# Performance work log

Measured on AMD Instinct MI355X. Metric: run time of the kernel, lower is better.

## Reference

```python
import jax, jax.numpy as jnp
import numpy as np

B, T, I, H = 256, 256, 2048, 128

def setup_inputs() -> dict:
    key = jax.random.key(0)
    ks = jax.random.split(key, 7)
    s = 1.0 / np.sqrt(H)  # torch RNN/Linear init scale
    return {
        "x": jax.random.normal(ks[0], (B, T, I), dtype=jnp.float32),
        "W_ih": jax.random.uniform(ks[1], (H, I), jnp.float32, -s, s),
        "W_hh": jax.random.uniform(ks[2], (H, H), jnp.float32, -s, s),
        "b_ih": jax.random.uniform(ks[3], (H,), jnp.float32, -s, s),
        "b_hh": jax.random.uniform(ks[4], (H,), jnp.float32, -s, s),
        "W_fc": jax.random.uniform(ks[5], (1, H), jnp.float32, -s, s),
        "b_fc": jax.random.uniform(ks[6], (1,), jnp.float32, -s, s),
    }

def reference(x, W_ih, W_hh, b_ih, b_hh, W_fc, b_fc):
    # Precompute input projection for all timesteps as one big GEMM: [B,T,H]
    xp = jnp.einsum('bti,hi->bth', x, W_ih) + (b_ih + b_hh)
    h0 = jnp.zeros((x.shape[0], W_hh.shape[0]), dtype=x.dtype)

    def step(h, xt):  # xt: [B,H]
        h = jnp.tanh(xt + h @ W_hh.T)
        return h, None

    hT, _ = jax.lax.scan(step, h0, jnp.swapaxes(xp, 0, 1))  # final hidden [B,H]
    out = hT @ W_fc.T + b_fc  # [B,1]
    return out.squeeze(1)     # [B]
```

## Files before the change

### kernel.cpp

```cpp
#include <hip/hip_runtime.h>
#include <hip/hip_bf16.h>
#include <math.h>

#define B_ 256
#define T_ 256
#define I_ 2048
#define H_ 128

#define BM 128
#define BK 32
#define NKT (I_ / BK)

typedef __attribute__((ext_vector_type(8))) short bf16x8;
typedef __attribute__((ext_vector_type(4))) float f32x4;
typedef _Float16 half2v __attribute__((ext_vector_type(2)));

static __device__ inline short f2bf(float f) {
    __hip_bfloat16 h = __float2bfloat16(f);
    return *reinterpret_cast<short*>(&h);
}

static __device__ inline bf16x8 pack8(float4 a, float4 b) {
    bf16x8 r;
    r[0] = f2bf(a.x); r[1] = f2bf(a.y); r[2] = f2bf(a.z); r[3] = f2bf(a.w);
    r[4] = f2bf(b.x); r[5] = f2bf(b.y); r[6] = f2bf(b.z); r[7] = f2bf(b.w);
    return r;
}

#define LGKM_BARRIER() do {                                  \
    asm volatile("s_waitcnt lgkmcnt(0)" ::: "memory");       \
    __builtin_amdgcn_sched_barrier(0);                       \
    __builtin_amdgcn_s_barrier();                            \
} while (0)

__global__ __launch_bounds__(256, 2) void proj_mfma(
    const float* __restrict__ x, const float* __restrict__ Wih,
    const float* __restrict__ bih, const float* __restrict__ bhh,
    float* __restrict__ xp)
{
    __shared__ __align__(16) float As[2][BM * BK];
    __shared__ __align__(16) float Bs[2][H_ * BK];

    const int tid  = threadIdx.x;
    const int lane = tid & 63;
    const int wid  = tid >> 6;
    const int wr   = wid >> 1;
    const int wc   = wid & 1;
    const long row0 = (long)blockIdx.x * BM;

    const int srow  = lane >> 3;
    const int sunit = (lane & 7) ^ srow;

    f32x4 acc[4][4];
    #pragma unroll
    for (int m = 0; m < 4; ++m)
        #pragma unroll
        for (int n = 0; n < 4; ++n)
            acc[m][n] = (f32x4){0.f, 0.f, 0.f, 0.f};

    const int fr = lane & 15;
    const int fq = lane >> 4;
    const int rb0 = wid * 32;

    #pragma unroll
    for (int i = 0; i < 4; ++i) {
        const int rbase = rb0 + i * 8;
        const float* ga = x   + (row0 + rbase + srow) * I_ + sunit * 4;
        const float* gb = Wih + (long)(rbase + srow) * I_ + sunit * 4;
        __builtin_amdgcn_global_load_lds(
            (const __attribute__((address_space(1))) void*)ga,
            (__attribute__((address_space(3))) void*)&As[0][rbase * BK], 16, 0, 0);
        __builtin_amdgcn_global_load_lds(
            (const __attribute__((address_space(1))) void*)gb,
            (__attribute__((address_space(3))) void*)&Bs[0][rbase * BK], 16, 0, 0);
    }
    __syncthreads();

    int p = 0;
    for (int t = 0; t < NKT; ++t) {
        if (t + 1 < NKT) {
            const int kk = (t + 1) * BK;
            #pragma unroll
            for (int i = 0; i < 4; ++i) {
                const int rbase = rb0 + i * 8;
                const float* ga = x   + (row0 + rbase + srow) * I_ + kk + sunit * 4;
                const float* gb = Wih + (long)(rbase + srow) * I_ + kk + sunit * 4;
                __builtin_amdgcn_global_load_lds(
                    (const __attribute__((address_space(1))) void*)ga,
                    (__attribute__((address_space(3))) void*)&As[p ^ 1][rbase * BK], 16, 0, 0);
                __builtin_amdgcn_global_load_lds(
                    (const __attribute__((address_space(1))) void*)gb,
                    (__attribute__((address_space(3))) void*)&Bs[p ^ 1][rbase * BK], 16, 0, 0);
            }
        }
        bf16x8 af[4], bfr[4];
        #pragma unroll
        for (int f = 0; f < 4; ++f) {
            const int ra_ = wr * 64 + f * 16 + fr;
            const float4 a0 = *reinterpret_cast<const float4*>(
                &As[p][ra_ * BK + (((fq * 2)     ^ (ra_ & 7)) * 4)]);
            const float4 a1 = *reinterpret_cast<const float4*>(
                &As[p][ra_ * BK + (((fq * 2 + 1) ^ (ra_ & 7)) * 4)]);
            af[f] = pack8(a0, a1);
            const int rb_ = wc * 64 + f * 16 + fr;
            const float4 b0 = *reinterpret_cast<const float4*>(
                &Bs[p][rb_ * BK + (((fq * 2)     ^ (rb_ & 7)) * 4)]);
            const float4 b1 = *reinterpret_cast<const float4*>(
                &Bs[p][rb_ * BK + (((fq * 2 + 1) ^ (rb_ & 7)) * 4)]);
            bfr[f] = pack8(b0, b1);
        }
        #pragma unroll
        for (int m = 0; m < 4; ++m)
            #pragma unroll
            for (int n = 0; n < 4; ++n)
                acc[m][n] = __builtin_amdgcn_mfma_f32_16x16x32_bf16(
                    af[m], bfr[n], acc[m][n], 0, 0, 0);
        __syncthreads();
        p ^= 1;
    }

    #pragma unroll
    for (int n = 0; n < 4; ++n) {
        const int col = wc * 64 + n * 16 + fr;
        const float bn = bih[col] + bhh[col];
        #pragma unroll
        for (int m = 0; m < 4; ++m) {
            const long rbase = row0 + wr * 64 + m * 16 + fq * 4;
            #pragma unroll
            for (int j = 0; j < 4; ++j)
                xp[(rbase + j) * H_ + col] = acc[m][n][j] + bn;
        }
    }
}

__global__ __launch_bounds__(256) void scan_kernel(
    const float* __restrict__ xp, const float* __restrict__ Whh,
    const float* __restrict__ Wfc, const float* __restrict__ bfc,
    float* __restrict__ out)
{
    __shared__ __align__(16) unsigned hpk[2][H_ / 2];

    const int tid  = threadIdx.x;
    const int lane = tid & 63;
    const int w    = tid >> 6;
    const int j    = w * 32 + (lane & 31);
    const int g    = lane >> 5;
    const int b    = blockIdx.x;

    half2v Wh[32];
    {
        const float4* wp = reinterpret_cast<const float4*>(&Whh[(long)j * H_ + g * 64]);
        #pragma unroll
        for (int q = 0; q < 16; ++q) {
            const float4 wv = wp[q];
            half2v p0, p1;
            p0[0] = (_Float16)wv.x; p0[1] = (_Float16)wv.y;
            p1[0] = (_Float16)wv.z; p1[1] = (_Float16)wv.w;
            Wh[2 * q]     = p0;
            Wh[2 * q + 1] = p1;
        }
    }
    if (tid < H_ / 2) hpk[0][tid] = 0u;

    const float* xprow = xp + (long)b * T_ * H_ + j;
    float xa = xprow[0 * H_];
    float xb = xprow[1 * H_];
    float xc = xprow[2 * H_];
    float xd = xprow[3 * H_];
    __syncthreads();

    auto body = [&](int t, float xpv) {
        const uint4* hp = reinterpret_cast<const uint4*>(&hpk[t & 1][g * 32]);
        float a0 = 0.f, a1 = 0.f, a2 = 0.f, a3 = 0.f;
        #pragma unroll
        for (int q = 0; q < 8; ++q) {
            const uint4 u = hp[q];
            a0 = __builtin_amdgcn_fdot2(__builtin_bit_cast(half2v, u.x), Wh[4*q+0], a0, false);
            a1 = __builtin_amdgcn_fdot2(__builtin_bit_cast(half2v, u.y), Wh[4*q+1], a1, false);
            a2 = __builtin_amdgcn_fdot2(__builtin_bit_cast(half2v, u.z), Wh[4*q+2], a2, false);
            a3 = __builtin_amdgcn_fdot2(__builtin_bit_cast(half2v, u.w), Wh[4*q+3], a3, false);
        }
        float part = (a0 + a1) + (a2 + a3);
        part += __shfl_xor(part, 32);
        const float pre = part + xpv;
        const float e = __expf(2.f * pre);
        const float h = 1.f - 2.f / (e + 1.f);
        if (g == 0) {
            reinterpret_cast<unsigned short*>(&hpk[(t + 1) & 1][0])[j] =
                __builtin_bit_cast(unsigned short, (_Float16)h);
        }
        LGKM_BARRIER();
    };

    for (int t = 0; t < T_; t += 4) {
        float xu;
        xu = xa; if (t + 4 < T_) xa = xprow[(long)(t + 4) * H_];
        body(t + 0, xu);
        xu = xb; if (t + 5 < T_) xb = xprow[(long)(t + 5) * H_];
        body(t + 1, xu);
        xu = xc; if (t + 6 < T_) xc = xprow[(long)(t + 6) * H_];
        body(t + 2, xu);
        xu = xd; if (t + 7 < T_) xd = xprow[(long)(t + 7) * H_];
        body(t + 3, xu);
    }

    if (w == 0) {
        const unsigned u = hpk[0][lane];
        const half2v hh = __builtin_bit_cast(half2v, u);
        float v = (float)hh[0] * Wfc[2 * lane] + (float)hh[1] * Wfc[2 * lane + 1];
        #pragma unroll
        for (int off = 32; off > 0; off >>= 1) v += __shfl_down(v, off);
        if (lane == 0) out[b] = v + bfc[0];
    }
}

extern "C" void kernel_launch(void* const* d_in, const int* in_sizes, int n_in,
                              void* d_out, int out_size, void* d_ws, size_t ws_size,
                              hipStream_t stream)
{
    const float* x   = (const float*)d_in[0];
    const float* Wih = (const float*)d_in[1];
    const float* Whh = (const float*)d_in[2];
    const float* bih = (const float*)d_in[3];
    const float* bhh = (const float*)d_in[4];
    const float* Wfc = (const float*)d_in[5];
    const float* bfc = (const float*)d_in[6];
    float* out = (float*)d_out;
    float* xp  = (float*)d_ws;

    proj_mfma<<<dim3((B_ * T_) / BM), dim3(256), 0, stream>>>(x, Wih, bih, bhh, xp);
    scan_kernel<<<dim3(B_), dim3(256), 0, stream>>>(xp, Whh, Wfc, bfc, out);
}
```

Baseline: 222.5 us.

## Pre-convert W_ih to bf16, triple-buffer GEMM loads, single-wave-per-row scan

A new kernel converts W_ih to bf16 once per call, so the projection GEMM loads half the B bytes and skips repacking B in its inner loop. The GEMM moves from double to triple buffering with explicit vmcnt waits and raw barriers, keeping two tiles in flight. Bias loads are hoisted to the start of the kernel. The scan kernel drops from 256 to 128 threads per block, with each thread doing a full 128-wide dot product and no cross-lane shuffle, at the cost of more registers and a longer serial chain per step.

```diff
diff --git a/kernel.cpp b/kernel.cpp
--- a/kernel.cpp
+++ b/kernel.cpp
@@ -10,6 +10,7 @@
 #define BM 128
 #define BK 32
 #define NKT (I_ / BK)
+#define NBUF 3
 
 typedef __attribute__((ext_vector_type(8))) short bf16x8;
 typedef __attribute__((ext_vector_type(4))) float f32x4;
@@ -33,13 +34,24 @@
     __builtin_amdgcn_s_barrier();                            \
 } while (0)
 
+static __device__ inline int sB(int r) { return (r & 3) ^ ((r >> 2) & 3); }
+
+__global__ __launch_bounds__(256) void convW(
+    const float* __restrict__ W, short* __restrict__ Wb)
+{
+    const int g = blockIdx.x * 256 + threadIdx.x;
+    const float4 v0 = reinterpret_cast<const float4*>(W)[2 * g];
+    const float4 v1 = reinterpret_cast<const float4*>(W)[2 * g + 1];
+    reinterpret_cast<bf16x8*>(Wb)[g] = pack8(v0, v1);
+}
+
 __global__ __launch_bounds__(256, 2) void proj_mfma(
-    const float* __restrict__ x, const float* __restrict__ Wih,
+    const float* __restrict__ x, const short* __restrict__ Wb,
     const float* __restrict__ bih, const float* __restrict__ bhh,
     float* __restrict__ xp)
 {
-    __shared__ __align__(16) float As[2][BM * BK];
-    __shared__ __align__(16) float Bs[2][H_ * BK];
+    __shared__ __align__(16) float As[NBUF][BM * BK];
+    __shared__ __align__(16) short Bs[NBUF][H_ * BK];
 
     const int tid  = threadIdx.x;
     const int lane = tid & 63;
@@ -48,8 +60,41 @@
     const int wc   = wid & 1;
     const long row0 = (long)blockIdx.x * BM;
 
+    const int fr = lane & 15;
+    const int fq = lane >> 4;
+
+    float biasr[4];
+    #pragma unroll
+    for (int n = 0; n < 4; ++n) {
+        const int col = wc * 64 + n * 16 + fr;
+        biasr[n] = bih[col] + bhh[col];
+    }
+
     const int srow  = lane >> 3;
-    const int sunit = (lane & 7) ^ srow;
+    const int sunitA = (lane & 7) ^ srow;
+    const int rb0 = wid * 32;
+    const int bu = lane & 3;
+
+    auto STAGE = [&](int tt, int buf) {
+        const int kk = tt * BK;
+        #pragma unroll
+        for (int i = 0; i < 4; ++i) {
+            const int rbase = rb0 + i * 8;
+            const float* ga = x + (row0 + rbase + srow) * I_ + kk + sunitA * 4;
+            __builtin_amdgcn_global_load_lds(
+                (const __attribute__((address_space(1))) void*)ga,
+                (__attribute__((address_space(3))) void*)&As[buf][rbase * BK], 16, 0, 0);
+        }
+        #pragma unroll
+        for (int i = 0; i < 2; ++i) {
+            const int brow = wid * 32 + i * 16 + (lane >> 2);
+            const int bswz = bu ^ sB(brow);
+            const short* gb = Wb + (long)brow * I_ + kk + bswz * 8;
+            __builtin_amdgcn_global_load_lds(
+                (const __attribute__((address_space(1))) void*)gb,
+                (__attribute__((address_space(3))) void*)&Bs[buf][(wid * 128 + i * 64) * 8], 16, 0, 0);
+        }
+    };
 
     f32x4 acc[4][4];
     #pragma unroll
@@ -58,41 +103,17 @@
         for (int n = 0; n < 4; ++n)
             acc[m][n] = (f32x4){0.f, 0.f, 0.f, 0.f};
 
-    const int fr = lane & 15;
-    const int fq = lane >> 4;
-    const int rb0 = wid * 32;
-
-    #pragma unroll
-    for (int i = 0; i < 4; ++i) {
-        const int rbase = rb0 + i * 8;
-        const float* ga = x   + (row0 + rbase + srow) * I_ + sunit * 4;
-        const float* gb = Wih + (long)(rbase + srow) * I_ + sunit * 4;
-        __builtin_amdgcn_global_load_lds(
-            (const __attribute__((address_space(1))) void*)ga,
-            (__attribute__((address_space(3))) void*)&As[0][rbase * BK], 16, 0, 0);
-        __builtin_amdgcn_global_load_lds(
-            (const __attribute__((address_space(1))) void*)gb,
-            (__attribute__((address_space(3))) void*)&Bs[0][rbase * BK], 16, 0, 0);
-    }
-    __syncthreads();
-
-    int p = 0;
+    STAGE(0, 0);
+    STAGE(1, 1);
+
     for (int t = 0; t < NKT; ++t) {
-        if (t + 1 < NKT) {
-            const int kk = (t + 1) * BK;
-            #pragma unroll
-            for (int i = 0; i < 4; ++i) {
-                const int rbase = rb0 + i * 8;
-                const float* ga = x   + (row0 + rbase + srow) * I_ + kk + sunit * 4;
-                const float* gb = Wih + (long)(rbase + srow) * I_ + kk + sunit * 4;
-                __builtin_amdgcn_global_load_lds(
-                    (const __attribute__((address_space(1))) void*)ga,
-                    (__attribute__((address_space(3))) void*)&As[p ^ 1][rbase * BK], 16, 0, 0);
-                __builtin_amdgcn_global_load_lds(
-                    (const __attribute__((address_space(1))) void*)gb,
-                    (__attribute__((address_space(3))) void*)&Bs[p ^ 1][rbase * BK], 16, 0, 0);
-            }
-        }
+        const int p = t % 3;
+        if (t == NKT - 1) { asm volatile("s_waitcnt vmcnt(0)" ::: "memory"); }
+        else              { asm volatile("s_waitcnt vmcnt(6)" ::: "memory"); }
+        __builtin_amdgcn_sched_barrier(0);
+        __builtin_amdgcn_s_barrier();
+        __builtin_amdgcn_sched_barrier(0);
+
         bf16x8 af[4], bfr[4];
         #pragma unroll
         for (int f = 0; f < 4; ++f) {
@@ -103,11 +124,8 @@
                 &As[p][ra_ * BK + (((fq * 2 + 1) ^ (ra_ & 7)) * 4)]);
             af[f] = pack8(a0, a1);
             const int rb_ = wc * 64 + f * 16 + fr;
-            const float4 b0 = *reinterpret_cast<const float4*>(
-                &Bs[p][rb_ * BK + (((fq * 2)     ^ (rb_ & 7)) * 4)]);
-            const float4 b1 = *reinterpret_cast<const float4*>(
-                &Bs[p][rb_ * BK + (((fq * 2 + 1) ^ (rb_ & 7)) * 4)]);
-            bfr[f] = pack8(b0, b1);
+            bfr[f] = *reinterpret_cast<const bf16x8*>(
+                &Bs[p][rb_ * 32 + ((fq ^ sB(rb_)) * 8)]);
         }
         #pragma unroll
         for (int m = 0; m < 4; ++m)
@@ -115,52 +133,49 @@
             for (int n = 0; n < 4; ++n)
                 acc[m][n] = __builtin_amdgcn_mfma_f32_16x16x32_bf16(
                     af[m], bfr[n], acc[m][n], 0, 0, 0);
-        __syncthreads();
-        p ^= 1;
+
+        __builtin_amdgcn_s_barrier();
+        __builtin_amdgcn_sched_barrier(0);
+        if (t + 2 < NKT) STAGE(t + 2, (t + 2) % 3);
     }
 
     #pragma unroll
     for (int n = 0; n < 4; ++n) {
         const int col = wc * 64 + n * 16 + fr;
-        const float bn = bih[col] + bhh[col];
         #pragma unroll
         for (int m = 0; m < 4; ++m) {
             const long rbase = row0 + wr * 64 + m * 16 + fq * 4;
             #pragma unroll
             for (int j = 0; j < 4; ++j)
-                xp[(rbase + j) * H_ + col] = acc[m][n][j] + bn;
-        }
-    }
-}
-
-__global__ __launch_bounds__(256) void scan_kernel(
+                xp[(rbase + j) * H_ + col] = acc[m][n][j] + biasr[n];
+        }
+    }
+}
+
+__global__ __launch_bounds__(128, 1) void scan_kernel(
     const float* __restrict__ xp, const float* __restrict__ Whh,
     const float* __restrict__ Wfc, const float* __restrict__ bfc,
     float* __restrict__ out)
 {
     __shared__ __align__(16) unsigned hpk[2][H_ / 2];
 
-    const int tid  = threadIdx.x;
-    const int lane = tid & 63;
-    const int w    = tid >> 6;
-    const int j    = w * 32 + (lane & 31);
-    const int g    = lane >> 5;
-    const int b    = blockIdx.x;
-
-    half2v Wh[32];
+    const int j = threadIdx.x;
+    const int b = blockIdx.x;
+
+    half2v W[64];
     {
-        const float4* wp = reinterpret_cast<const float4*>(&Whh[(long)j * H_ + g * 64]);
-        #pragma unroll
-        for (int q = 0; q < 16; ++q) {
+        const float4* wp = reinterpret_cast<const float4*>(&Whh[(long)j * H_]);
+        #pragma unroll
+        for (int q = 0; q < 32; ++q) {
             const float4 wv = wp[q];
             half2v p0, p1;
             p0[0] = (_Float16)wv.x; p0[1] = (_Float16)wv.y;
             p1[0] = (_Float16)wv.z; p1[1] = (_Float16)wv.w;
-            Wh[2 * q]     = p0;
-            Wh[2 * q + 1] = p1;
-        }
-    }
-    if (tid < H_ / 2) hpk[0][tid] = 0u;
+            W[2 * q]     = p0;
+            W[2 * q + 1] = p1;
+        }
+    }
+    if (j < H_ / 2) hpk[0][j] = 0u;
 
     const float* xprow = xp + (long)b * T_ * H_ + j;
     float xa = xprow[0 * H_];
@@ -170,25 +185,21 @@
     __syncthreads();
 
     auto body = [&](int t, float xpv) {
-        const uint4* hp = reinterpret_cast<const uint4*>(&hpk[t & 1][g * 32]);
+        const uint4* hp = reinterpret_cast<const uint4*>(&hpk[t & 1][0]);
         float a0 = 0.f, a1 = 0.f, a2 = 0.f, a3 = 0.f;
         #pragma unroll
-        for (int q = 0; q < 8; ++q) {
+        for (int q = 0; q < 16; ++q) {
             const uint4 u = hp[q];
-            a0 = __builtin_amdgcn_fdot2(__builtin_bit_cast(half2v, u.x), Wh[4*q+0], a0, false);
-            a1 = __builtin_amdgcn_fdot2(__builtin_bit_cast(half2v, u.y), Wh[4*q+1], a1, false);
-            a2 = __builtin_amdgcn_fdot2(__builtin_bit_cast(half2v, u.z), Wh[4*q+2], a2, false);
-            a3 = __builtin_amdgcn_fdot2(__builtin_bit_cast(half2v, u.w), Wh[4*q+3], a3, false);
-        }
-        float part = (a0 + a1) + (a2 + a3);
-        part += __shfl_xor(part, 32);
-        const float pre = part + xpv;
+            a0 = __builtin_amdgcn_fdot2(__builtin_bit_cast(half2v, u.x), W[4*q+0], a0, false);
+            a1 = __builtin_amdgcn_fdot2(__builtin_bit_cast(half2v, u.y), W[4*q+1], a1, false);
+            a2 = __builtin_amdgcn_fdot2(__builtin_bit_cast(half2v, u.z), W[4*q+2], a2, false);
+            a3 = __builtin_amdgcn_fdot2(__builtin_bit_cast(half2v, u.w), W[4*q+3], a3, false);
+        }
+        const float pre = ((a0 + a1) + (a2 + a3)) + xpv;
         const float e = __expf(2.f * pre);
         const float h = 1.f - 2.f / (e + 1.f);
-        if (g == 0) {
-            reinterpret_cast<unsigned short*>(&hpk[(t + 1) & 1][0])[j] =
-                __builtin_bit_cast(unsigned short, (_Float16)h);
-        }
+        reinterpret_cast<unsigned short*>(&hpk[(t + 1) & 1][0])[j] =
+            __builtin_bit_cast(unsigned short, (_Float16)h);
         LGKM_BARRIER();
     };
 
@@ -204,13 +215,14 @@
         body(t + 3, xu);
     }
 
-    if (w == 0) {
-        const unsigned u = hpk[0][lane];
+    if (j < 64) {
+        const unsigned u = hpk[0][j];
         const half2v hh = __builtin_bit_cast(half2v, u);
-        float v = (float)hh[0] * Wfc[2 * lane] + (float)hh[1] * Wfc[2 * lane + 1];
+        const float2 wf = reinterpret_cast<const float2*>(Wfc)[j];
+        float v = (float)hh[0] * wf.x + (float)hh[1] * wf.y;
         #pragma unroll
         for (int off = 32; off > 0; off >>= 1) v += __shfl_down(v, off);
-        if (lane == 0) out[b] = v + bfc[0];
+        if (j == 0) out[b] = v + bfc[0];
     }
 }
 
@@ -227,7 +239,9 @@
     const float* bfc = (const float*)d_in[6];
     float* out = (float*)d_out;
     float* xp  = (float*)d_ws;
-
-    proj_mfma<<<dim3((B_ * T_) / BM), dim3(256), 0, stream>>>(x, Wih, bih, bhh, xp);
-    scan_kernel<<<dim3(B_), dim3(256), 0, stream>>>(xp, Whh, Wfc, bfc, out);
-}
+    short* Wb  = (short*)((char*)d_ws + (size_t)B_ * T_ * H_ * sizeof(float));
+
+    convW<<<dim3((H_ * I_) / (256 * 8)), dim3(256), 0, stream>>>(Wih, Wb);
+    proj_mfma<<<dim3((B_ * T_) / BM), dim3(256), 0, stream>>>(x, Wb, bih, bhh, xp);
+    scan_kernel<<<dim3(B_), dim3(128), 0, stream>>>(xp, Whh, Wfc, bfc, out);
+}
```

Result: slower. 241.0 us (+8.3%).
